# Kernel tuning notes

Measured on AMD Instinct MI355X. Metric: run time of the kernel, lower is better.

The kernel has to match this reference:

```python
import jax, jax.numpy as jnp
import numpy as np

C64 = jnp.complex64
I2 = jnp.eye(2, dtype=C64)
X = jnp.array([[0, 1], [1, 0]], dtype=C64)


def rz(t):
    e = jnp.exp(-0.5j * t.astype(jnp.complex64))
    return jnp.diag(jnp.stack([e, jnp.conj(e)]))


def rx(t):
    c = jnp.cos(0.5 * t).astype(C64)
    s = (-1j * jnp.sin(0.5 * t)).astype(C64)
    return jnp.stack([jnp.stack([c, s]), jnp.stack([s, c])])


def ctrl(g):
    # |0><0| x I + |1><1| x g  (control = first wire, target = second, adjacent)
    z = jnp.zeros((2, 2), dtype=C64)
    return jnp.block([[I2, z], [z, g]])


def embed(g, wire, n):
    # place gate g (on `wire`..`wire+k-1`, wire 0 = MSB as in PennyLane) into n-qubit space
    k = int(np.log2(g.shape[0]))
    return jnp.kron(jnp.kron(jnp.eye(2 ** wire, dtype=C64), g),
                    jnp.eye(2 ** (n - wire - k), dtype=C64))


def qft_mat(n):
    N = 2 ** n
    j = np.arange(N)
    return jnp.asarray(np.exp(2j * np.pi * np.outer(j, j) / N) / np.sqrt(N), dtype=np.complex64)


def z_signs(wire, n):
    idx = np.arange(2 ** n)
    return jnp.asarray(1.0 - 2.0 * ((idx >> (n - 1 - wire)) & 1), dtype=np.float32)


def build_U1(f1, p1):
    n = 4
    Q = qft_mat(n)
    gates = [Q]
    for i in range(n):
        gates.append(embed(rz(f1[i]), i, n))
    gates.append(Q.conj().T)
    gates += [embed(ctrl(rz(p1[0])), 0, n), embed(X, 0, n),
              embed(ctrl(rx(p1[1])), 0, n), embed(X, 0, n),
              embed(ctrl(rz(p1[0])), 2, n), embed(X, 2, n),
              embed(ctrl(rx(p1[1])), 2, n), embed(X, 2, n)]
    U = jnp.eye(2 ** n, dtype=C64)
    for g in gates:
        U = g @ U
    return U


def build_U2(f2, p2):
    n = 2
    Q = qft_mat(n)
    gates = [Q, embed(rz(f2[0]), 0, n), embed(rz(f2[1]), 1, n), Q.conj().T,
             embed(ctrl(rz(p2[0])), 0, n), embed(X, 0, n),
             embed(ctrl(rx(p2[1])), 0, n), embed(X, 0, n)]
    U = jnp.eye(2 ** n, dtype=C64)
    for g in gates:
        U = g @ U
    return U


def setup_inputs() -> dict:
    key = jax.random.key(0)
    ks = jax.random.split(key, 7)
    B = 524288
    return {
        "x": jax.random.normal(ks[0], (B, 1, 4, 4), dtype=jnp.float32),
        "f1": jax.random.normal(ks[1], (4,), dtype=jnp.float32),
        "p1": jax.random.normal(ks[2], (2,), dtype=jnp.float32),
        "f2": jax.random.normal(ks[3], (2,), dtype=jnp.float32),
        "p2": jax.random.normal(ks[4], (2,), dtype=jnp.float32),
        "W": jax.random.normal(ks[5], (2, 1), dtype=jnp.float32),
        "b": jax.random.normal(ks[6], (2,), dtype=jnp.float32),
    }


def reference(x, f1, p1, f2, p2, W, b):
    B = x.shape[0]
    # ----- layer 1: AmplitudeEmbedding (normalized) on 4 qubits -----
    xf = x.reshape(B, 16)
    psi = (xf / jnp.linalg.norm(xf, axis=1, keepdims=True)).astype(C64)  # [B,16]
    U1 = build_U1(f1, p1)                                                 # [16,16]
    psi = psi @ U1.T
    probs = psi.real ** 2 + psi.imag ** 2                                 # [B,16]
    e1 = probs @ z_signs(1, 4)   # <Z_1>
    e3 = probs @ z_signs(3, 4)   # <Z_3>
    # ----- layer 2: AngleEmbedding(RY) on 2 qubits -----
    a = jnp.stack([e1, e3], axis=-1)                                      # [B,2]
    c, s = jnp.cos(0.5 * a), jnp.sin(0.5 * a)
    psi2 = jnp.stack([c[:, 0] * c[:, 1], c[:, 0] * s[:, 1],
                      s[:, 0] * c[:, 1], s[:, 0] * s[:, 1]], axis=-1).astype(C64)  # [B,4]
    U2 = build_U2(f2, p2)
    psi2 = psi2 @ U2.T
    probs2 = psi2.real ** 2 + psi2.imag ** 2
    e = probs2 @ z_signs(1, 2)                                            # [B]
    # ----- classical head -----
    logits = e[:, None] @ W.T + b                                         # [B,2]
    return logits
```

## Files before the change

kernel.cpp:

```cpp
#include <hip/hip_runtime.h>
#include <math.h>

#define PI_F 3.14159265358979323846f

__global__ void setup_kernel(const float* __restrict__ f1,
                             const float* __restrict__ p1,
                             const float* __restrict__ f2,
                             const float* __restrict__ p2,
                             const float* __restrict__ W,
                             const float* __restrict__ bb,
                             float* __restrict__ ws)
{
    __shared__ float2 M[256];
    __shared__ float2 tab[16];
    __shared__ float2 M2[16];

    const int t = threadIdx.x;
    const int r = t >> 4, c = t & 15;

    if (t < 16) {
        float ang = (2.0f * PI_F / 16.0f) * (float)t;
        tab[t] = make_float2(cosf(ang), sinf(ang));
    }
    M[t] = make_float2((r == c) ? 1.0f : 0.0f, 0.0f);
    __syncthreads();

    {
        float2 acc = make_float2(0.0f, 0.0f);
        for (int k = 0; k < 16; ++k) {
            float2 w = tab[(r * k) & 15];
            float2 v = M[k * 16 + c];
            acc.x += w.x * v.x - w.y * v.y;
            acc.y += w.x * v.y + w.y * v.x;
        }
        acc.x *= 0.25f; acc.y *= 0.25f;
        __syncthreads();
        M[t] = acc;
        __syncthreads();
    }
    for (int i = 0; i < 4; ++i) {
        float th = f1[i];
        float ch = cosf(0.5f * th), sh = sinf(0.5f * th);
        int bit = (r >> (3 - i)) & 1;
        float2 d = make_float2(ch, bit ? sh : -sh);
        float2 m = M[t];
        M[t] = make_float2(d.x * m.x - d.y * m.y, d.x * m.y + d.y * m.x);
        __syncthreads();
    }
    {
        float2 acc = make_float2(0.0f, 0.0f);
        for (int k = 0; k < 16; ++k) {
            float2 w = tab[(r * k) & 15];
            float2 v = M[k * 16 + c];
            acc.x += w.x * v.x + w.y * v.y;
            acc.y += w.x * v.y - w.y * v.x;
        }
        acc.x *= 0.25f; acc.y *= 0.25f;
        __syncthreads();
        M[t] = acc;
        __syncthreads();
    }
    for (int w2 = 0; w2 <= 2; w2 += 2) {
        const int mc = 1 << (3 - w2);
        const int mt = mc >> 1;
        {
            float th = p1[0];
            float ch = cosf(0.5f * th), sh = sinf(0.5f * th);
            float2 d = (r & mc) ? make_float2(ch, (r & mt) ? sh : -sh)
                                : make_float2(1.0f, 0.0f);
            float2 m = M[t];
            M[t] = make_float2(d.x * m.x - d.y * m.y, d.x * m.y + d.y * m.x);
            __syncthreads();
        }
        {
            float2 v = M[(r ^ mc) * 16 + c];
            __syncthreads();
            M[t] = v;
            __syncthreads();
        }
        {
            float th = p1[1];
            float ch = cosf(0.5f * th), sh = sinf(0.5f * th);
            float2 own = M[t];
            float2 par = M[(r ^ mt) * 16 + c];
            __syncthreads();
            float2 nv;
            if (r & mc) {
                nv.x = ch * own.x + sh * par.y;
                nv.y = ch * own.y - sh * par.x;
            } else {
                nv = own;
            }
            M[t] = nv;
            __syncthreads();
        }
        {
            float2 v = M[(r ^ mc) * 16 + c];
            __syncthreads();
            M[t] = v;
            __syncthreads();
        }
    }

    {
        float q1 = 0.0f, q3 = 0.0f;
        for (int k = 0; k < 16; ++k) {
            float2 a  = M[k * 16 + r];
            float2 bv = M[k * 16 + c];
            float d = a.x * bv.x + a.y * bv.y;
            q1 += ((k >> 2) & 1) ? -d : d;
            q3 += (k & 1) ? -d : d;
        }
        if (r <= c) {
            int p = r * 16 - (r * (r - 1)) / 2 + (c - r);
            float sc = (r == c) ? 1.0f : 2.0f;
            ws[2 * p]     = sc * q1;
            ws[2 * p + 1] = sc * q3;
        }
    }

    const bool act = (t < 16);
    const int r2 = t >> 2, c2 = t & 3;
    if (act) M2[t] = make_float2((r2 == c2) ? 1.0f : 0.0f, 0.0f);
    __syncthreads();

    {
        float2 acc = make_float2(0.0f, 0.0f);
        if (act) {
            for (int k = 0; k < 4; ++k) {
                int m = (r2 * k) & 3;
                float2 w = (m == 0) ? make_float2(1, 0) :
                           (m == 1) ? make_float2(0, 1) :
                           (m == 2) ? make_float2(-1, 0) : make_float2(0, -1);
                float2 v = M2[k * 4 + c2];
                acc.x += w.x * v.x - w.y * v.y;
                acc.y += w.x * v.y + w.y * v.x;
            }
            acc.x *= 0.5f; acc.y *= 0.5f;
        }
        __syncthreads();
        if (act) M2[t] = acc;
        __syncthreads();
    }
    for (int i = 0; i < 2; ++i) {
        float th = f2[i];
        float ch = cosf(0.5f * th), sh = sinf(0.5f * th);
        if (act) {
            int bit = (r2 >> (1 - i)) & 1;
            float2 d = make_float2(ch, bit ? sh : -sh);
            float2 m = M2[t];
            M2[t] = make_float2(d.x * m.x - d.y * m.y, d.x * m.y + d.y * m.x);
        }
        __syncthreads();
    }
    {
        float2 acc = make_float2(0.0f, 0.0f);
        if (act) {
            for (int k = 0; k < 4; ++k) {
                int m = (r2 * k) & 3;
                float2 w = (m == 0) ? make_float2(1, 0) :
                           (m == 1) ? make_float2(0, 1) :
                           (m == 2) ? make_float2(-1, 0) : make_float2(0, -1);
                float2 v = M2[k * 4 + c2];
                acc.x += w.x * v.x + w.y * v.y;
                acc.y += w.x * v.y - w.y * v.x;
            }
            acc.x *= 0.5f; acc.y *= 0.5f;
        }
        __syncthreads();
        if (act) M2[t] = acc;
        __syncthreads();
    }
    {
        float th = p2[0];
        float ch = cosf(0.5f * th), sh = sinf(0.5f * th);
        if (act) {
            float2 d = (r2 & 2) ? make_float2(ch, (r2 & 1) ? sh : -sh)
                                : make_float2(1.0f, 0.0f);
            float2 m = M2[t];
            M2[t] = make_float2(d.x * m.x - d.y * m.y, d.x * m.y + d.y * m.x);
        }
        __syncthreads();
    }
    {
        float2 v = make_float2(0.0f, 0.0f);
        if (act) v = M2[((r2 ^ 2) * 4) + c2];
        __syncthreads();
        if (act) M2[t] = v;
        __syncthreads();
    }
    {
        float th = p2[1];
        float ch = cosf(0.5f * th), sh = sinf(0.5f * th);
        float2 nv = make_float2(0.0f, 0.0f);
        if (act) {
            float2 own = M2[t];
            float2 par = M2[((r2 ^ 1) * 4) + c2];
            if (r2 & 2) {
                nv.x = ch * own.x + sh * par.y;
                nv.y = ch * own.y - sh * par.x;
            } else {
                nv = own;
            }
        }
        __syncthreads();
        if (act) M2[t] = nv;
        __syncthreads();
    }
    {
        float2 v = make_float2(0.0f, 0.0f);
        if (act) v = M2[((r2 ^ 2) * 4) + c2];
        __syncthreads();
        if (act) M2[t] = v;
        __syncthreads();
    }
    if (act) {
        float q2v = 0.0f;
        for (int k = 0; k < 4; ++k) {
            float2 a  = M2[k * 4 + r2];
            float2 bv = M2[k * 4 + c2];
            float d = a.x * bv.x + a.y * bv.y;
            q2v += (k & 1) ? -d : d;
        }
        if (r2 <= c2) {
            int p = r2 * 4 - (r2 * (r2 - 1)) / 2 + (c2 - r2);
            ws[272 + p] = ((r2 == c2) ? 1.0f : 2.0f) * q2v;
        }
    }
    if (t == 0) {
        ws[282] = W[0];
        ws[283] = W[1];
        ws[284] = bb[0];
        ws[285] = bb[1];
    }
}

__global__ __launch_bounds__(256) void qfcn_main(const float* __restrict__ x,
                                                 const float* __restrict__ q,
                                                 float* __restrict__ out,
                                                 int B)
{
    int row = blockIdx.x * 256 + threadIdx.x;
    if (row >= B) return;

    const float4* xp = reinterpret_cast<const float4*>(x + (size_t)row * 16);
    float4 a0 = xp[0], a1 = xp[1], a2 = xp[2], a3 = xp[3];
    float xs[16] = {a0.x, a0.y, a0.z, a0.w, a1.x, a1.y, a1.z, a1.w,
                    a2.x, a2.y, a2.z, a2.w, a3.x, a3.y, a3.z, a3.w};

    float ss = 0.0f;
#pragma unroll
    for (int i = 0; i < 16; ++i) ss = fmaf(xs[i], xs[i], ss);

    float e1 = 0.0f, e3 = 0.0f;
    int p = 0;
#pragma unroll
    for (int i = 0; i < 16; ++i) {
#pragma unroll
        for (int j = i; j < 16; ++j) {
            float tp = xs[i] * xs[j];
            e1 = fmaf(q[2 * p],     tp, e1);
            e3 = fmaf(q[2 * p + 1], tp, e3);
            ++p;
        }
    }
    float inv = __builtin_amdgcn_rcpf(ss);
    e1 *= inv;
    e3 *= inv;

    float s0 = __sinf(0.5f * e1), c0 = __cosf(0.5f * e1);
    float s1 = __sinf(0.5f * e3), c1 = __cosf(0.5f * e3);
    float vv[4] = {c0 * c1, c0 * s1, s0 * c1, s0 * s1};

    float e = 0.0f;
    int pp = 0;
#pragma unroll
    for (int i = 0; i < 4; ++i) {
#pragma unroll
        for (int j = i; j < 4; ++j) {
            e = fmaf(q[272 + pp], vv[i] * vv[j], e);
            ++pp;
        }
    }
    float2 o;
    o.x = fmaf(e, q[282], q[284]);
    o.y = fmaf(e, q[283], q[285]);
    reinterpret_cast<float2*>(out)[row] = o;
}

extern "C" void kernel_launch(void* const* d_in, const int* in_sizes, int n_in,
                              void* d_out, int out_size, void* d_ws, size_t ws_size,
                              hipStream_t stream)
{
    const float* x  = (const float*)d_in[0];
    const float* f1 = (const float*)d_in[1];
    const float* p1 = (const float*)d_in[2];
    const float* f2 = (const float*)d_in[3];
    const float* p2 = (const float*)d_in[4];
    const float* W  = (const float*)d_in[5];
    const float* bb = (const float*)d_in[6];
    float* out = (float*)d_out;
    float* ws  = (float*)d_ws;

    int B = in_sizes[0] / 16;

    hipLaunchKernelGGL(setup_kernel, dim3(1), dim3(256), 0, stream,
                       f1, p1, f2, p2, W, bb, ws);
    int blocks = (B + 255) / 256;
    hipLaunchKernelGGL(qfcn_main, dim3(blocks), dim3(256), 0, stream,
                       x, ws, out, B);
}
```

Baseline: 94.60 us.

## Fuse setup into main kernel, recomputing circuit coefficients per block in LDS

Removes the separate single-block setup launch and the workspace round trip. Every block of the main kernel now rebuilds the 16x16 and 4x4 circuit matrices and their quadratic-form coefficients in shared memory, then uses them from LDS. This drops one launch and the serial dependency on a tiny kernel. In exchange it adds redundant per-block work (several matrix products and barriers) across 2048 blocks, plus LDS reads in the inner loop instead of scalar loads of uniform values.

After: 97.65 us. +3.2%, slower.

```diff
diff --git a/kernel.cpp b/kernel.cpp
--- a/kernel.cpp
+++ b/kernel.cpp
@@ -3,17 +3,19 @@
 
 #define PI_F 3.14159265358979323846f
 
-__global__ void setup_kernel(const float* __restrict__ f1,
-                             const float* __restrict__ p1,
-                             const float* __restrict__ f2,
-                             const float* __restrict__ p2,
-                             const float* __restrict__ W,
-                             const float* __restrict__ bb,
-                             float* __restrict__ ws)
+__global__ __launch_bounds__(256) void qfcn_fused(
+    const float* __restrict__ x,
+    const float* __restrict__ f1, const float* __restrict__ p1,
+    const float* __restrict__ f2, const float* __restrict__ p2,
+    const float* __restrict__ W,  const float* __restrict__ bb,
+    float* __restrict__ out, int B)
 {
     __shared__ float2 M[256];
     __shared__ float2 tab[16];
     __shared__ float2 M2[16];
+    __shared__ float2 qq[136];
+    __shared__ float  q2s[10];
+    __shared__ float  wb[4];
 
     const int t = threadIdx.x;
     const int r = t >> 4, c = t & 15;
@@ -114,8 +116,7 @@
         if (r <= c) {
             int p = r * 16 - (r * (r - 1)) / 2 + (c - r);
             float sc = (r == c) ? 1.0f : 2.0f;
-            ws[2 * p]     = sc * q1;
-            ws[2 * p + 1] = sc * q3;
+            qq[p] = make_float2(sc * q1, sc * q3);
         }
     }
 
@@ -224,23 +225,15 @@
         }
         if (r2 <= c2) {
             int p = r2 * 4 - (r2 * (r2 - 1)) / 2 + (c2 - r2);
-            ws[272 + p] = ((r2 == c2) ? 1.0f : 2.0f) * q2v;
+            q2s[p] = ((r2 == c2) ? 1.0f : 2.0f) * q2v;
         }
     }
     if (t == 0) {
-        ws[282] = W[0];
-        ws[283] = W[1];
-        ws[284] = bb[0];
-        ws[285] = bb[1];
-    }
-}
-
-__global__ __launch_bounds__(256) void qfcn_main(const float* __restrict__ x,
-                                                 const float* __restrict__ q,
-                                                 float* __restrict__ out,
-                                                 int B)
-{
-    int row = blockIdx.x * 256 + threadIdx.x;
+        wb[0] = W[0]; wb[1] = W[1]; wb[2] = bb[0]; wb[3] = bb[1];
+    }
+    __syncthreads();
+
+    int row = blockIdx.x * 256 + t;
     if (row >= B) return;
 
     const float4* xp = reinterpret_cast<const float4*>(x + (size_t)row * 16);
@@ -258,9 +251,10 @@
     for (int i = 0; i < 16; ++i) {
 #pragma unroll
         for (int j = i; j < 16; ++j) {
+            float2 ab = qq[p];
             float tp = xs[i] * xs[j];
-            e1 = fmaf(q[2 * p],     tp, e1);
-            e3 = fmaf(q[2 * p + 1], tp, e3);
+            e1 = fmaf(ab.x, tp, e1);
+            e3 = fmaf(ab.y, tp, e3);
             ++p;
         }
     }
@@ -278,13 +272,13 @@
     for (int i = 0; i < 4; ++i) {
 #pragma unroll
         for (int j = i; j < 4; ++j) {
-            e = fmaf(q[272 + pp], vv[i] * vv[j], e);
+            e = fmaf(q2s[pp], vv[i] * vv[j], e);
             ++pp;
         }
     }
     float2 o;
-    o.x = fmaf(e, q[282], q[284]);
-    o.y = fmaf(e, q[283], q[285]);
+    o.x = fmaf(e, wb[0], wb[2]);
+    o.y = fmaf(e, wb[1], wb[3]);
     reinterpret_cast<float2*>(out)[row] = o;
 }
 
@@ -300,13 +294,9 @@
     const float* W  = (const float*)d_in[5];
     const float* bb = (const float*)d_in[6];
     float* out = (float*)d_out;
-    float* ws  = (float*)d_ws;
 
     int B = in_sizes[0] / 16;
-
-    hipLaunchKernelGGL(setup_kernel, dim3(1), dim3(256), 0, stream,
-                       f1, p1, f2, p2, W, bb, ws);
     int blocks = (B + 255) / 256;
-    hipLaunchKernelGGL(qfcn_main, dim3(blocks), dim3(256), 0, stream,
-                       x, ws, out, B);
+    hipLaunchKernelGGL(qfcn_fused, dim3(blocks), dim3(256), 0, stream,
+                       x, f1, p1, f2, p2, W, bb, out, B);
 }
```
